# Optimization experiments

Hardware: AMD Instinct MI355X
Metric: run time of the kernel (lower is better)

## Reference

```python
import jax, jax.numpy as jnp
import numpy as np

PEP_LEN = 15
IN_CH = 512
OUT_CH = 512
BATCH = 8192


def setup_inputs() -> dict:
    key = jax.random.key(0)
    k_x, k_w = jax.random.split(key)
    peptide_x = jax.random.normal(k_x, (BATCH, PEP_LEN, IN_CH), dtype=jnp.float32)
    # truncated_normal_(std=0.02) init; plain normal*0.02 is fine for a numeric reference
    weight = jax.random.normal(k_w, (PEP_LEN, IN_CH, OUT_CH), dtype=jnp.float32) * 0.02
    bias = jnp.zeros((PEP_LEN, OUT_CH), dtype=jnp.float32)
    return {"peptide_x": peptide_x, "weight": weight, "bias": bias}


def reference(peptide_x, weight, bias) -> jnp.ndarray:
    # Original torch code does a full tensordot over all pep_len positions
    # ([B,P,P,O]) then gathers the diagonal. That is mathematically identical
    # to a per-position batched matmul, which we compute directly.
    out = jnp.einsum('bpi,pio->bpo', peptide_x, weight)  # [B, P, O]
    return out + bias  # bias broadcasts over batch
```

## Files before the change

kernel.cpp:

```cpp
#include <hip/hip_runtime.h>
#include <hip/hip_bf16.h>
#include <stdint.h>

#define BATCH 8192
#define PEP 15
#define INC 512
#define OUTC 512
#define XROW (PEP*INC)
#define WT_P_ELEMS (INC*OUTC)
#define NSTEPS 16

typedef float f32x4 __attribute__((ext_vector_type(4)));
typedef short s16x8 __attribute__((ext_vector_type(8)));
typedef unsigned int u32x4 __attribute__((ext_vector_type(4)));

__device__ __forceinline__ ushort f2b(float v) {
  uint u = __float_as_uint(v);
  u += 0x7fffu + ((u >> 16) & 1u);
  return (ushort)(u >> 16);
}

__device__ __forceinline__ uint cvtpk(float a, float b) {
  uint r;
  asm("v_cvt_pk_bf16_f32 %0, %1, %2" : "=v"(r) : "v"(a), "v"(b));
  return r;
}

__global__ __launch_bounds__(256) void wt_kernel(const float* __restrict__ w,
                                                 ushort* __restrict__ wt) {
  __shared__ float tile[32 * 133];
  const int t = threadIdx.x;
  const int bid = blockIdx.x;
  const int nchunk = bid & 3;
  const int ks     = (bid >> 2) & 15;
  const int p      = bid >> 6;

  const float* src = w + (size_t)p * WT_P_ELEMS + (size_t)(ks * 32) * OUTC + nchunk * 128;
  const int rk = t >> 5;
  const int rc = (t & 31) * 4;
#pragma unroll
  for (int i = 0; i < 4; ++i) {
    const int k = rk + i * 8;
    f32x4 v = *(const f32x4*)(src + (size_t)k * OUTC + rc);
    *(f32x4*)&tile[k * 133 + rc] = v;
  }
  __syncthreads();

  ushort* dst = wt + ((size_t)(p * 16 + ks) * 32 + nchunk * 8) * 512;
#pragma unroll
  for (int h = 0; h < 2; ++h) {
    const int f   = t + h * 256;
    const int n16 = f >> 6;
    const int l   = f & 63;
    const int fr  = l & 15;
    const int g   = l >> 4;
    s16x8 hv;
#pragma unroll
    for (int e = 0; e < 8; ++e)
      hv[e] = (short)f2b(tile[(g * 8 + e) * 133 + n16 * 16 + fr]);
    *(s16x8*)(dst + (size_t)n16 * 512 + l * 8) = hv;
  }
}

__global__ __launch_bounds__(512, 4) void gemm_kernel(const float* __restrict__ x,
                                                      const ushort* __restrict__ wt,
                                                      const float* __restrict__ bias,
                                                      float* __restrict__ out) {
  __shared__ __align__(16) char lds_raw[49152];
  typedef ushort AshT[8][64][8];
  typedef ushort BshT[16][64][8];
  AshT* Ash = (AshT*)lds_raw;
  BshT* Bsh = (BshT*)(lds_raw + 16384);

  const int t    = threadIdx.x;
  const int lane = t & 63;
  const int wid  = t >> 6;
  const int wm   = wid >> 2;
  const int wn   = wid & 3;
  const int fr   = lane & 15;
  const int g    = lane >> 4;

  const int bid  = blockIdx.x;
  const int xcd  = bid & 7;
  const int j    = bid >> 3;
  const int n2   = j & 1;
  const int pair = xcd * 120 + (j >> 1);
  const int mb   = pair & 63;
  const int p    = pair >> 6;
  const int m0   = mb * 128;

  const float* asrc = x + (size_t)(m0 + wid * 16 + fr) * XROW + p * INC + g * 8;
  const ushort* bsrc = wt + (size_t)p * WT_P_ELEMS
                     + (size_t)(n2 * 16 + wid * 2) * 512 + (size_t)lane * 8;

  f32x4 acc[4][4] = {};
  f32x4 pa0, pa1;

  auto cvt_store = [&](int buf) {
    u32x4 aw;
    aw[0] = cvtpk(pa0[0], pa0[1]); aw[1] = cvtpk(pa0[2], pa0[3]);
    aw[2] = cvtpk(pa1[0], pa1[1]); aw[3] = cvtpk(pa1[2], pa1[3]);
    *(u32x4*)&Ash[buf][wid][lane][0] = aw;
  };
  auto stageB = [&](int ks, int buf) {
#pragma unroll
    for (int q = 0; q < 2; ++q) {
      __builtin_amdgcn_global_load_lds(
          (const __attribute__((address_space(1))) void*)(bsrc + (size_t)ks * 16384 + q * 512),
          (__attribute__((address_space(3))) void*)(&Bsh[buf][wid * 2 + q][lane][0]),
          16, 0, 0);
    }
  };

  pa0 = *(const f32x4*)(asrc);
  pa1 = *(const f32x4*)(asrc + 4);
  cvt_store(0);
  stageB(0, 0);
  pa0 = *(const f32x4*)(asrc + 32);
  pa1 = *(const f32x4*)(asrc + 36);
  __syncthreads();

#pragma unroll
  for (int ks = 0; ks < NSTEPS; ++ks) {
    const int cur = ks & 1;
    const int nxt = cur ^ 1;

    if (ks + 1 < NSTEPS) {
      cvt_store(nxt);
      stageB(ks + 1, nxt);
    }
    if (ks + 2 < NSTEPS) {
      pa0 = *(const f32x4*)(asrc + (ks + 2) * 32);
      pa1 = *(const f32x4*)(asrc + (ks + 2) * 32 + 4);
    }

    s16x8 af[4];
#pragma unroll
    for (int i = 0; i < 4; ++i)
      af[i] = *(const s16x8*)&Ash[cur][wm * 4 + i][lane][0];

    s16x8 bf[4];
#pragma unroll
    for (int nf = 0; nf < 4; ++nf)
      bf[nf] = *(const s16x8*)&Bsh[cur][wn * 4 + nf][lane][0];

#pragma unroll
    for (int i = 0; i < 4; ++i)
#pragma unroll
      for (int nf = 0; nf < 4; ++nf)
        acc[i][nf] = __builtin_amdgcn_mfma_f32_16x16x32_bf16(af[i], bf[nf], acc[i][nf], 0, 0, 0);

    __syncthreads();
  }

  const int n0q = wn * 64;
  float bv[4];
#pragma unroll
  for (int nf = 0; nf < 4; ++nf) bv[nf] = bias[p * OUTC + n2 * 256 + n0q + nf * 16 + fr];

  float* reg0 = (float*)lds_raw;
  float* reg1 = (float*)lds_raw + 16 * 260;
  float* myreg = wm ? reg1 : reg0;
  const float* obase = out + p * INC + n2 * 256 + lane * 4;

#pragma unroll
  for (int s = 0; s < 4; ++s) {
    __builtin_amdgcn_sched_barrier(0);
#pragma unroll
    for (int nf = 0; nf < 4; ++nf)
#pragma unroll
      for (int r = 0; r < 4; ++r)
        myreg[(g * 4 + r) * 260 + n0q + nf * 16 + fr] = acc[s][nf][r] + bv[nf];
    __builtin_amdgcn_sched_barrier(0);
    asm volatile("s_waitcnt lgkmcnt(0)" ::: "memory");
    __builtin_amdgcn_s_barrier();
    __builtin_amdgcn_sched_barrier(0);

#pragma unroll
    for (int pass = 0; pass < 4; ++pass) {
      const int row_id = pass * 8 + wid;
      const int rgn = row_id >> 4;
      const int rw  = row_id & 15;
      f32x4 v = *(const f32x4*)((rgn ? reg1 : reg0) + rw * 260 + lane * 4);
      __builtin_nontemporal_store(v,
          (f32x4*)((float*)obase + (size_t)(m0 + rgn * 64 + s * 16 + rw) * XROW));
    }
    __builtin_amdgcn_sched_barrier(0);
    asm volatile("s_waitcnt lgkmcnt(0)" ::: "memory");
    __builtin_amdgcn_s_barrier();
    __builtin_amdgcn_sched_barrier(0);
  }
}

__global__ void naive_kernel(const float* __restrict__ x, const float* __restrict__ w,
                             const float* __restrict__ bias, float* __restrict__ out) {
  size_t i = (size_t)blockIdx.x * 256 + threadIdx.x;
  if (i >= (size_t)BATCH * PEP * OUTC) return;
  int o  = (int)(i & (OUTC - 1));
  int pp = (int)((i >> 9) % PEP);
  size_t b = i / ((size_t)PEP * OUTC);
  const float* xr = x + b * XROW + pp * INC;
  const float* wc = w + (size_t)pp * INC * OUTC + o;
  float s = bias[pp * OUTC + o];
  for (int k = 0; k < INC; ++k) s += xr[k] * wc[(size_t)k * OUTC];
  out[i] = s;
}

extern "C" void kernel_launch(void* const* d_in, const int* in_sizes, int n_in,
                              void* d_out, int out_size, void* d_ws, size_t ws_size,
                              hipStream_t stream) {
  const float* x    = (const float*)d_in[0];
  const float* w    = (const float*)d_in[1];
  const float* bias = (const float*)d_in[2];
  float* out = (float*)d_out;

  const size_t wt_bytes = (size_t)PEP * INC * OUTC * sizeof(ushort);
  if (ws_size >= wt_bytes) {
    wt_kernel<<<960, 256, 0, stream>>>(w, (ushort*)d_ws);
    gemm_kernel<<<1920, 512, 0, stream>>>(x, (const ushort*)d_ws, bias, out);
  } else {
    size_t total = (size_t)BATCH * PEP * OUTC;
    naive_kernel<<<(int)((total + 255) / 256), 256, 0, stream>>>(x, w, bias, out);
  }
}
```

Before: 148.8 us.

## Deepen GEMM pipeline with 64-wide K steps and triple-buffered B in dynamic LDS

The GEMM main loop now covers K in 8 steps of 64 instead of 16 steps of 32. B tiles are triple-buffered in a 128 KB dynamic LDS allocation, and A is prefetched two steps ahead through a register ring. Explicit vmcnt/lgkmcnt waits and raw barriers replace __syncthreads, and s_setprio raises priority around the MFMA block. The aim is to hide global load latency and halve the barriers per tile. In exchange, the larger LDS footprint cuts resident blocks per CU (launch bounds drop to 2), so there is less wave-level parallelism to cover the memory-heavy fp32 input and output traffic.

```diff
diff --git a/kernel.cpp b/kernel.cpp
--- a/kernel.cpp
+++ b/kernel.cpp
@@ -8,7 +8,7 @@
 #define OUTC 512
 #define XROW (PEP*INC)
 #define WT_P_ELEMS (INC*OUTC)
-#define NSTEPS 16
+#define NSTEPS 8
 
 typedef float f32x4 __attribute__((ext_vector_type(4)));
 typedef short s16x8 __attribute__((ext_vector_type(8)));
@@ -62,15 +62,13 @@
   }
 }
 
-__global__ __launch_bounds__(512, 4) void gemm_kernel(const float* __restrict__ x,
+__global__ __launch_bounds__(512, 2) void gemm_kernel(const float* __restrict__ x,
                                                       const ushort* __restrict__ wt,
                                                       const float* __restrict__ bias,
                                                       float* __restrict__ out) {
-  __shared__ __align__(16) char lds_raw[49152];
-  typedef ushort AshT[8][64][8];
-  typedef ushort BshT[16][64][8];
-  AshT* Ash = (AshT*)lds_raw;
-  BshT* Bsh = (BshT*)(lds_raw + 16384);
+  extern __shared__ __align__(16) char lds_raw[];
+  auto Ash = (ushort (*)[8][2][64][8])lds_raw;
+  auto Bsh = (ushort (*)[2][16][64][8])(lds_raw + 32768);
 
   const int t    = threadIdx.x;
   const int lane = t & 63;
@@ -90,67 +88,93 @@
   const int m0   = mb * 128;
 
   const float* asrc = x + (size_t)(m0 + wid * 16 + fr) * XROW + p * INC + g * 8;
-  const ushort* bsrc = wt + (size_t)p * WT_P_ELEMS
-                     + (size_t)(n2 * 16 + wid * 2) * 512 + (size_t)lane * 8;
+  const ushort* wt_p = wt + (size_t)p * WT_P_ELEMS + (size_t)lane * 8;
 
   f32x4 acc[4][4] = {};
-  f32x4 pa0, pa1;
-
-  auto cvt_store = [&](int buf) {
-    u32x4 aw;
-    aw[0] = cvtpk(pa0[0], pa0[1]); aw[1] = cvtpk(pa0[2], pa0[3]);
-    aw[2] = cvtpk(pa1[0], pa1[1]); aw[3] = cvtpk(pa1[2], pa1[3]);
-    *(u32x4*)&Ash[buf][wid][lane][0] = aw;
+  f32x4 pa[2][2][2];
+
+  auto load_pa = [&](int ks, int ring) {
+#pragma unroll
+    for (int ksub = 0; ksub < 2; ++ksub) {
+      pa[ring][ksub][0] = *(const f32x4*)(asrc + ks * 64 + ksub * 32);
+      pa[ring][ksub][1] = *(const f32x4*)(asrc + ks * 64 + ksub * 32 + 4);
+    }
+  };
+  auto cvt_store = [&](int ring, int buf) {
+#pragma unroll
+    for (int ksub = 0; ksub < 2; ++ksub) {
+      u32x4 aw;
+      aw[0] = cvtpk(pa[ring][ksub][0][0], pa[ring][ksub][0][1]);
+      aw[1] = cvtpk(pa[ring][ksub][0][2], pa[ring][ksub][0][3]);
+      aw[2] = cvtpk(pa[ring][ksub][1][0], pa[ring][ksub][1][1]);
+      aw[3] = cvtpk(pa[ring][ksub][1][2], pa[ring][ksub][1][3]);
+      *(u32x4*)&Ash[buf][wid][ksub][lane][0] = aw;
+    }
   };
   auto stageB = [&](int ks, int buf) {
 #pragma unroll
-    for (int q = 0; q < 2; ++q) {
+    for (int q = 0; q < 4; ++q) {
+      const int c    = wid * 4 + q;
+      const int ksb  = c >> 4;
+      const int n16l = c & 15;
       __builtin_amdgcn_global_load_lds(
-          (const __attribute__((address_space(1))) void*)(bsrc + (size_t)ks * 16384 + q * 512),
-          (__attribute__((address_space(3))) void*)(&Bsh[buf][wid * 2 + q][lane][0]),
+          (const __attribute__((address_space(1))) void*)
+            (wt_p + ((size_t)(ks * 2 + ksb) * 32 + n2 * 16 + n16l) * 512),
+          (__attribute__((address_space(3))) void*)(&Bsh[buf][ksb][n16l][lane][0]),
           16, 0, 0);
     }
   };
 
-  pa0 = *(const f32x4*)(asrc);
-  pa1 = *(const f32x4*)(asrc + 4);
-  cvt_store(0);
+  load_pa(0, 0);
+  __builtin_amdgcn_sched_barrier(0);
   stageB(0, 0);
-  pa0 = *(const f32x4*)(asrc + 32);
-  pa1 = *(const f32x4*)(asrc + 36);
-  __syncthreads();
+  __builtin_amdgcn_sched_barrier(0);
+  stageB(1, 1);
+  __builtin_amdgcn_sched_barrier(0);
+  load_pa(1, 1);
+  __builtin_amdgcn_sched_barrier(0);
+  cvt_store(0, 0);
+  __builtin_amdgcn_sched_barrier(0);
+  asm volatile("s_waitcnt vmcnt(8)" ::: "memory");
+  asm volatile("s_waitcnt lgkmcnt(0)" ::: "memory");
+  __builtin_amdgcn_s_barrier();
+  __builtin_amdgcn_sched_barrier(0);
 
 #pragma unroll
   for (int ks = 0; ks < NSTEPS; ++ks) {
-    const int cur = ks & 1;
-    const int nxt = cur ^ 1;
-
-    if (ks + 1 < NSTEPS) {
-      cvt_store(nxt);
-      stageB(ks + 1, nxt);
-    }
     if (ks + 2 < NSTEPS) {
-      pa0 = *(const f32x4*)(asrc + (ks + 2) * 32);
-      pa1 = *(const f32x4*)(asrc + (ks + 2) * 32 + 4);
-    }
-
-    s16x8 af[4];
-#pragma unroll
-    for (int i = 0; i < 4; ++i)
-      af[i] = *(const s16x8*)&Ash[cur][wm * 4 + i][lane][0];
-
-    s16x8 bf[4];
-#pragma unroll
-    for (int nf = 0; nf < 4; ++nf)
-      bf[nf] = *(const s16x8*)&Bsh[cur][wn * 4 + nf][lane][0];
-
-#pragma unroll
-    for (int i = 0; i < 4; ++i)
+      load_pa(ks + 2, ks & 1);
+      stageB(ks + 2, (ks + 2) % 3);
+    }
+    __builtin_amdgcn_sched_barrier(0);
+
+    if (ks + 1 < NSTEPS) cvt_store((ks + 1) & 1, (ks + 1) & 1);
+    __builtin_amdgcn_sched_barrier(0);
+
+    __builtin_amdgcn_s_setprio(1);
+#pragma unroll
+    for (int ksub = 0; ksub < 2; ++ksub) {
+      s16x8 af[4], bf[4];
+#pragma unroll
+      for (int i = 0; i < 4; ++i)
+        af[i] = *(const s16x8*)&Ash[ks & 1][wm * 4 + i][ksub][lane][0];
 #pragma unroll
       for (int nf = 0; nf < 4; ++nf)
-        acc[i][nf] = __builtin_amdgcn_mfma_f32_16x16x32_bf16(af[i], bf[nf], acc[i][nf], 0, 0, 0);
-
-    __syncthreads();
+        bf[nf] = *(const s16x8*)&Bsh[ks % 3][ksub][wn * 4 + nf][lane][0];
+#pragma unroll
+      for (int i = 0; i < 4; ++i)
+#pragma unroll
+        for (int nf = 0; nf < 4; ++nf)
+          acc[i][nf] = __builtin_amdgcn_mfma_f32_16x16x32_bf16(af[i], bf[nf], acc[i][nf], 0, 0, 0);
+    }
+    __builtin_amdgcn_s_setprio(0);
+    __builtin_amdgcn_sched_barrier(0);
+
+    if (ks < 6)       asm volatile("s_waitcnt vmcnt(8)" ::: "memory");
+    else if (ks == 6) asm volatile("s_waitcnt vmcnt(0)" ::: "memory");
+    asm volatile("s_waitcnt lgkmcnt(0)" ::: "memory");
+    __builtin_amdgcn_s_barrier();
+    __builtin_amdgcn_sched_barrier(0);
   }
 
   const int n0q = wn * 64;
@@ -215,9 +239,15 @@
   float* out = (float*)d_out;
 
   const size_t wt_bytes = (size_t)PEP * INC * OUTC * sizeof(ushort);
-  if (ws_size >= wt_bytes) {
+  static int lds_ok = -1;
+  if (lds_ok < 0) {
+    hipError_t e = hipFuncSetAttribute(reinterpret_cast<const void*>(gemm_kernel),
+                                       hipFuncAttributeMaxDynamicSharedMemorySize, 131072);
+    lds_ok = (e == hipSuccess) ? 1 : 0;
+  }
+  if (ws_size >= wt_bytes && lds_ok == 1) {
     wt_kernel<<<960, 256, 0, stream>>>(w, (ushort*)d_ws);
-    gemm_kernel<<<1920, 512, 0, stream>>>(x, (const ushort*)d_ws, bias, out);
+    gemm_kernel<<<1920, 512, 131072, stream>>>(x, (const ushort*)d_ws, bias, out);
   } else {
     size_t total = (size_t)BATCH * PEP * OUTC;
     naive_kernel<<<(int)((total + 255) / 256), 256, 0, stream>>>(x, w, bias, out);
```

Result: slower. 170.8 us (+14.8%).

## Triple-buffer B tiles with explicit vmcnt waits and MFMA priority boost

Applied to the files above, without the earlier changes.

Moves the B operand staging to a three-slot LDS ring that prefetches two k-steps ahead, replacing __syncthreads with manual s_waitcnt vmcnt/lgkmcnt counts and raw barriers under sched_barrier fences. MFMA blocks are wrapped in s_setprio to favour compute issue. The goal is to hide global-to-LDS latency for the weight tiles more deeply. LDS grows from 48 KB to 64 KB per block, which can lower occupancy, and the hand-counted vmcnt values must match the real number of outstanding loads or results go wrong.

```diff
diff --git a/kernel.cpp b/kernel.cpp
--- a/kernel.cpp
+++ b/kernel.cpp
@@ -66,11 +66,9 @@
                                                       const ushort* __restrict__ wt,
                                                       const float* __restrict__ bias,
                                                       float* __restrict__ out) {
-  __shared__ __align__(16) char lds_raw[49152];
-  typedef ushort AshT[8][64][8];
-  typedef ushort BshT[16][64][8];
-  AshT* Ash = (AshT*)lds_raw;
-  BshT* Bsh = (BshT*)(lds_raw + 16384);
+  __shared__ __align__(16) char lds_raw[65536];
+  auto Ash = (ushort (*)[8][64][8])lds_raw;
+  auto Bsh = (ushort (*)[16][64][8])(lds_raw + 16384);
 
   const int t    = threadIdx.x;
   const int lane = t & 63;
@@ -115,42 +113,57 @@
   pa0 = *(const f32x4*)(asrc);
   pa1 = *(const f32x4*)(asrc + 4);
   cvt_store(0);
-  stageB(0, 0);
+  __builtin_amdgcn_sched_barrier(0);
   pa0 = *(const f32x4*)(asrc + 32);
   pa1 = *(const f32x4*)(asrc + 36);
-  __syncthreads();
+  __builtin_amdgcn_sched_barrier(0);
+  stageB(0, 0);
+  stageB(1, 1);
+  __builtin_amdgcn_sched_barrier(0);
+  asm volatile("s_waitcnt vmcnt(2)" ::: "memory");
+  asm volatile("s_waitcnt lgkmcnt(0)" ::: "memory");
+  __builtin_amdgcn_s_barrier();
+  __builtin_amdgcn_sched_barrier(0);
 
 #pragma unroll
   for (int ks = 0; ks < NSTEPS; ++ks) {
-    const int cur = ks & 1;
-    const int nxt = cur ^ 1;
-
-    if (ks + 1 < NSTEPS) {
-      cvt_store(nxt);
-      stageB(ks + 1, nxt);
-    }
+    const int cur  = ks & 1;
+    const int curB = ks % 3;
+
+    if (ks + 1 < NSTEPS) cvt_store((ks + 1) & 1);
+    __builtin_amdgcn_sched_barrier(0);
+
     if (ks + 2 < NSTEPS) {
       pa0 = *(const f32x4*)(asrc + (ks + 2) * 32);
       pa1 = *(const f32x4*)(asrc + (ks + 2) * 32 + 4);
     }
-
-    s16x8 af[4];
+    __builtin_amdgcn_sched_barrier(0);
+
+    if (ks + 2 < NSTEPS) stageB(ks + 2, (ks + 2) % 3);
+    __builtin_amdgcn_sched_barrier(0);
+
+    s16x8 af[4], bf[4];
 #pragma unroll
     for (int i = 0; i < 4; ++i)
       af[i] = *(const s16x8*)&Ash[cur][wm * 4 + i][lane][0];
-
-    s16x8 bf[4];
 #pragma unroll
     for (int nf = 0; nf < 4; ++nf)
-      bf[nf] = *(const s16x8*)&Bsh[cur][wn * 4 + nf][lane][0];
-
+      bf[nf] = *(const s16x8*)&Bsh[curB][wn * 4 + nf][lane][0];
+
+    __builtin_amdgcn_s_setprio(1);
 #pragma unroll
     for (int i = 0; i < 4; ++i)
 #pragma unroll
       for (int nf = 0; nf < 4; ++nf)
         acc[i][nf] = __builtin_amdgcn_mfma_f32_16x16x32_bf16(af[i], bf[nf], acc[i][nf], 0, 0, 0);
-
-    __syncthreads();
+    __builtin_amdgcn_s_setprio(0);
+    __builtin_amdgcn_sched_barrier(0);
+
+    if (ks <= 13)      asm volatile("s_waitcnt vmcnt(4)" ::: "memory");
+    else if (ks == 14) asm volatile("s_waitcnt vmcnt(0)" ::: "memory");
+    asm volatile("s_waitcnt lgkmcnt(0)" ::: "memory");
+    __builtin_amdgcn_s_barrier();
+    __builtin_amdgcn_sched_barrier(0);
   }
 
   const int n0q = wn * 64;
```

Measured after the change: 144.7 us. 2.7% less time.
